# Performance work log

Hardware: AMD Instinct MI355X
Metric: run time of the kernel (lower is better)

The kernel has to match this reference:

```python
import jax, jax.numpy as jnp
import numpy as np

N = 8192; S = 32; EMB = 256; NH = 8; HD = EMB // NH; NT = 4; K = 2; L = 2; E = 131072
IN_DIMS = [128, 64, 32, 16]; COUNTS = [4096, 2048, 1024, 1024]
BETA = 1.0; TEMPER = 1.0; SLOPE = 0.2; LN_EPS = 1e-5


def setup_inputs() -> dict:
    key = jax.random.key(0)
    ks = iter(jax.random.split(key, 64))
    def nrm(shape, scale=1.0):
        return jax.random.normal(next(ks), shape, jnp.float32) * scale
    inp = {}
    for i, (d, c) in enumerate(zip(IN_DIMS, COUNTS)):
        inp[f"feat{i}"] = nrm((c, d))
        inp[f"Wfc{i}"] = nrm((d, EMB), d ** -0.5)
        inp[f"bfc{i}"] = nrm((EMB,), 0.01)
    inp["type_emb"] = nrm((NT, NT))
    inp["Wgcn"] = nrm((K, EMB, EMB), EMB ** -0.5)
    inp["bgcn"] = nrm((K, EMB), 0.01)
    inp["Wre"] = nrm((K, NT, NT), NT ** -0.5)
    inp["bre"] = nrm((K, NT), 0.01)
    inp["wtre"] = jnp.ones((K, NT), jnp.float32)
    inp["Wl"] = nrm((L, EMB, EMB), EMB ** -0.5)
    inp["Wr"] = nrm((L, EMB, EMB), EMB ** -0.5)
    inp["al"] = nrm((L, HD), HD ** -0.5)
    inp["ar"] = nrm((L, HD), HD ** -0.5)
    inp["Wrs"] = nrm((L, NT, NT * NH), NT ** -0.5)
    inp["Wrt"] = nrm((L, NT, NT * NH), NT ** -0.5)
    inp["Wfin"] = nrm((L, EMB, EMB), EMB ** -0.5)
    inp["ln_g"] = jnp.ones((L, EMB), jnp.float32)
    inp["ln_b"] = jnp.zeros((L, EMB), jnp.float32)
    inp["src"] = jax.random.randint(next(ks), (E,), 0, N)
    inp["dst"] = jax.random.randint(next(ks), (E,), 0, N)
    inp["node_type"] = jnp.concatenate([jnp.full((c,), t, jnp.int32) for t, c in enumerate(COUNTS)])
    inp["seqs"] = jax.random.randint(next(ks), (N, S), 0, N)
    return inp


def _l2n(x):
    return x / jnp.maximum(jnp.linalg.norm(x, axis=1, keepdims=True), 1e-12)


def _ln(x, g, b):
    m = x.mean(-1, keepdims=True)
    v = ((x - m) ** 2).mean(-1, keepdims=True)
    return (x - m) * jax.lax.rsqrt(v + LN_EPS) * g + b


def _agt(h, rh, Wl_, Wr_, al_, ar_, Wrs_, Wrt_, Wfin_, g_, b_):
    B, Sq, _ = h.shape
    fl = (h @ Wl_).reshape(B, Sq, NH, HD).transpose(0, 2, 1, 3)  # [B,NH,S,HD]
    fr = (h @ Wr_).reshape(B, Sq, NH, HD).transpose(0, 2, 1, 3)
    sl = jnp.einsum('bhsd,d->bhs', jax.nn.leaky_relu(fl, SLOPE), al_)
    sr = jnp.einsum('bhsd,d->bhs', jax.nn.leaky_relu(fr, SLOPE), ar_)
    score = sl[:, :, :, None] + sr[:, :, None, :]  # [B,NH,S,S]
    rk = (rh @ Wrs_).reshape(B, Sq, NH, NT).transpose(0, 2, 1, 3)  # [B,NH,S,NT]
    rq = (rh @ Wrt_).reshape(B, Sq, NH, NT).transpose(0, 2, 1, 3)
    score = score + BETA * jnp.einsum('bhir,bhjr->bhij', rk, rq)
    attn = jax.nn.softmax(score / TEMPER, axis=-1)
    ctx = jnp.einsum('bhij,bhjd->bhid', attn, fr)
    h_sa = ctx.transpose(0, 2, 1, 3).reshape(B, Sq, EMB)
    return _ln(h + h_sa @ Wfin_, g_, b_)


def reference(feat0, feat1, feat2, feat3, Wfc0, bfc0, Wfc1, bfc1, Wfc2, bfc2, Wfc3, bfc3,
              type_emb, Wgcn, bgcn, Wre, bre, wtre, Wl, Wr, al, ar, Wrs, Wrt, Wfin, ln_g, ln_b,
              src, dst, node_type, seqs):
    feats = [feat0, feat1, feat2, feat3]
    Wfcs = [Wfc0, Wfc1, Wfc2, Wfc3]
    bfcs = [bfc0, bfc1, bfc2, bfc3]
    gh = jnp.concatenate([f @ W + b for f, W, b in zip(feats, Wfcs, bfcs)], axis=0)  # [N,EMB]
    Nn = gh.shape[0]
    loop = jnp.arange(Nn, dtype=src.dtype)  # self-loops (graph.add_self_loop)
    src_f = jnp.concatenate([src, loop]); dst_f = jnp.concatenate([dst, loop])
    ones = jnp.ones(src_f.shape[0], jnp.float32)
    outdeg = jnp.clip(jax.ops.segment_sum(ones, src_f, num_segments=Nn), 1.0)
    indeg = jnp.clip(jax.ops.segment_sum(ones, dst_f, num_segments=Nn), 1.0)
    n_out = outdeg ** -0.5; n_in = indeg ** -0.5
    ret = [_l2n(gh)]
    R = type_emb[node_type]  # [N,NT]
    for k in range(K):
        # GraphConv, norm='both', relu
        x = (gh * n_out[:, None]) @ Wgcn[k]
        gh = jax.nn.relu(jax.ops.segment_sum(x[src_f], dst_f, num_segments=Nn) * n_in[:, None] + bgcn[k])
        # REConv: left norm, weight, per-node type scale, scatter-sum, right norm, bias, relu
        r = ((R * n_out[:, None]) @ Wre[k]) * wtre[k][node_type][:, None]
        R = jax.nn.relu(jax.ops.segment_sum(r[src_f], dst_f, num_segments=Nn) * n_in[:, None] + bre[k])
    h = gh[seqs]   # [N,S,EMB]
    rh = R[seqs]   # [N,S,NT]
    for l in range(L):
        h = _agt(h, rh, Wl[l], Wr[l], al[l], ar[l], Wrs[l], Wrt[l], Wfin[l], ln_g[l], ln_b[l])
        ret.append(_l2n(h[:, 0, :]))
    return jnp.concatenate(ret, axis=1)  # [N, EMB*(1+L)]
```

## Files before the change

### kernel.cpp

```cpp
#include <hip/hip_runtime.h>
#include <hip/hip_bf16.h>
#include <cstdint>
#include <cstddef>

typedef unsigned short ushortT;
typedef unsigned int uintT;

using bf16x8 = __attribute__((ext_vector_type(8))) short;
using f32x4  = __attribute__((ext_vector_type(4))) float;

static constexpr int NN  = 8192;
static constexpr int EE  = 131072;
static constexpr float SLOPE  = 0.2f;
static constexpr float LN_EPS = 1e-5f;

#define DEVI __device__ __forceinline__

DEVI float red32(float v) {
  #pragma unroll
  for (int m = 16; m >= 1; m >>= 1) v += __shfl_xor(v, m, 64);
  return v;
}
DEVI float red64(float v) {
  #pragma unroll
  for (int m = 32; m >= 1; m >>= 1) v += __shfl_xor(v, m, 64);
  return v;
}
DEVI float max32(float v) {
  #pragma unroll
  for (int m = 16; m >= 1; m >>= 1) v = fmaxf(v, __shfl_xor(v, m, 64));
  return v;
}
DEVI float blo(uintT u) { union { uintT i; float f; } c; c.i = u << 16; return c.f; }
DEVI float bhi(uintT u) { union { uintT i; float f; } c; c.i = u & 0xffff0000u; return c.f; }
DEVI float b2f(ushortT u) { union { uintT i; float f; } c; c.i = ((uintT)u) << 16; return c.f; }
DEVI ushortT f2bu(float f) {
  __hip_bfloat16 h = __float2bfloat16(f);
  return *reinterpret_cast<ushortT*>(&h);
}
DEVI void storeC(float* p, float v) { *p = v; }
DEVI void storeC(ushortT* p, float v) { *p = f2bu(v); }

__global__ __launch_bounds__(256) void fc_kernel(
    const float* __restrict__ f0, const float* __restrict__ f1,
    const float* __restrict__ f2, const float* __restrict__ f3,
    const float* __restrict__ w0, const float* __restrict__ w1,
    const float* __restrict__ w2, const float* __restrict__ w3,
    const float* __restrict__ b0, const float* __restrict__ b1,
    const float* __restrict__ b2, const float* __restrict__ b3,
    float* __restrict__ gh, float* __restrict__ out)
{
  const int nb = blockIdx.x * 32;
  const int t  = threadIdx.x;
  int base, D;
  const float *F, *W, *Bv;
  if (nb < 4096)      { base = 0;    D = 128; F = f0; W = w0; Bv = b0; }
  else if (nb < 6144) { base = 4096; D = 64;  F = f1; W = w1; Bv = b1; }
  else if (nb < 7168) { base = 6144; D = 32;  F = f2; W = w2; Bv = b2; }
  else                { base = 7168; D = 16;  F = f3; W = w3; Bv = b3; }

  __shared__ float Fs[32 * 128];
  __shared__ float red[32][4];
  __shared__ float nrm[32];

  const int total = 32 * D;
  for (int i = t; i < total; i += 256) Fs[i] = F[(size_t)(nb - base) * D + i];
  __syncthreads();

  float acc[32];
  #pragma unroll
  for (int r = 0; r < 32; ++r) acc[r] = Bv[t];
  for (int d = 0; d < D; ++d) {
    float w = W[(size_t)d * 256 + t];
    #pragma unroll
    for (int r = 0; r < 32; ++r) acc[r] = fmaf(Fs[r * D + d], w, acc[r]);
  }

  const int lane = t & 63, wid = t >> 6;
  #pragma unroll
  for (int r = 0; r < 32; ++r) {
    float v = acc[r] * acc[r];
    for (int o = 32; o > 0; o >>= 1) v += __shfl_down(v, o, 64);
    if (lane == 0) red[r][wid] = v;
  }
  __syncthreads();
  if (t < 32) {
    float s = red[t][0] + red[t][1] + red[t][2] + red[t][3];
    nrm[t] = 1.0f / fmaxf(sqrtf(s), 1e-12f);
  }
  __syncthreads();
  #pragma unroll
  for (int r = 0; r < 32; ++r) {
    gh[(size_t)(nb + r) * 256 + t]  = acc[r];
    out[(size_t)(nb + r) * 768 + t] = acc[r] * nrm[r];
  }
}

__global__ __launch_bounds__(256) void zero_counts(int* outc, int* inc) {
  int g = blockIdx.x * 256 + threadIdx.x;
  if (g < NN) outc[g] = 0; else inc[g - NN] = 0;
}
__global__ __launch_bounds__(256) void count_deg(const int* __restrict__ src,
                                                 const int* __restrict__ dst,
                                                 int* outc, int* inc) {
  int g = blockIdx.x * 256 + threadIdx.x;
  atomicAdd(&outc[src[g]], 1);
  atomicAdd(&inc[dst[g]], 1);
}
__global__ __launch_bounds__(1024) void scan_kernel(
    const int* __restrict__ inc, const int* __restrict__ outc,
    int* __restrict__ offs, int* __restrict__ cur,
    float* __restrict__ n_out, float* __restrict__ n_in)
{
  __shared__ int sums[1024];
  const int t = threadIdx.x;
  int x[8];
  const int base = t * 8;
  int s = 0;
  #pragma unroll
  for (int i = 0; i < 8; ++i) { int v = inc[base + i] + 1; x[i] = s; s += v; }
  sums[t] = s;
  __syncthreads();
  for (int off = 1; off < 1024; off <<= 1) {
    int a = (t >= off) ? sums[t - off] : 0;
    __syncthreads();
    sums[t] += a;
    __syncthreads();
  }
  const int pre = (t > 0) ? sums[t - 1] : 0;
  #pragma unroll
  for (int i = 0; i < 8; ++i) {
    const int o = pre + x[i];
    offs[base + i] = o;
    cur[base + i]  = o;
    n_in[base + i]  = rsqrtf((float)inc[base + i] + 1.0f);
    n_out[base + i] = rsqrtf((float)outc[base + i] + 1.0f);
  }
  if (t == 1023) offs[NN] = sums[1023];
}
__global__ __launch_bounds__(256) void fill_csr(const int* __restrict__ src,
                                                const int* __restrict__ dst,
                                                int* cur, int* __restrict__ csr) {
  int g = blockIdx.x * 256 + threadIdx.x;
  int s, d;
  if (g < EE) { s = src[g]; d = dst[g]; }
  else        { s = g - EE; d = g - EE; }
  int pos = atomicAdd(&cur[d], 1);
  csr[pos] = s;
}
__global__ __launch_bounds__(256) void init_R(const float* __restrict__ type_emb,
                                              const int* __restrict__ nt,
                                              float* __restrict__ R) {
  int g = blockIdx.x * 256 + threadIdx.x;
  int n = g >> 2, c = g & 3;
  R[g] = type_emb[nt[n] * 4 + c];
}

template<bool ROWSCALE, bool STORE, bool RED, typename CT>
__global__ __launch_bounds__(256) void mfma_gemm_kernel(
    const float* __restrict__ A, const float* __restrict__ W,
    const float* __restrict__ rowscale,
    CT* __restrict__ C, const float* __restrict__ avec,
    float* __restrict__ SSo)
{
  const int m0 = blockIdx.x * 64;
  const int n0 = blockIdx.y * 64;
  const int t = threadIdx.x;
  const int w = t >> 6, l = t & 63;
  const int wr = w >> 1, wc = w & 1;
  const int l15 = l & 15, l16 = l >> 4;

  __shared__ alignas(16) ushortT As[64][72];
  __shared__ alignas(16) ushortT Bs[64][72];

  f32x4 acc[2][2];
  #pragma unroll
  for (int mh = 0; mh < 2; ++mh)
    #pragma unroll
    for (int nh = 0; nh < 2; ++nh)
      #pragma unroll
      for (int r = 0; r < 4; ++r) acc[mh][nh][r] = 0.f;

  for (int k0 = 0; k0 < 256; k0 += 64) {
    #pragma unroll
    for (int rep = 0; rep < 16; ++rep) {
      int flat = rep * 256 + t;
      int r = flat >> 6, k = flat & 63;
      float v = A[(size_t)(m0 + r) * 256 + k0 + k];
      if constexpr (ROWSCALE) v *= rowscale[m0 + r];
      As[r][k] = f2bu(v);
    }
    #pragma unroll
    for (int rep = 0; rep < 16; ++rep) {
      int flat = rep * 256 + t;
      int k = flat >> 6, n = flat & 63;
      Bs[n][k] = f2bu(W[(size_t)(k0 + k) * 256 + n0 + n]);
    }
    __syncthreads();
    #pragma unroll
    for (int ks = 0; ks < 2; ++ks) {
      const int kb = ks * 32 + l16 * 8;
      bf16x8 afr[2], bfr[2];
      #pragma unroll
      for (int mh = 0; mh < 2; ++mh)
        afr[mh] = *reinterpret_cast<const bf16x8*>(&As[wr * 32 + mh * 16 + l15][kb]);
      #pragma unroll
      for (int nh = 0; nh < 2; ++nh)
        bfr[nh] = *reinterpret_cast<const bf16x8*>(&Bs[wc * 32 + nh * 16 + l15][kb]);
      #pragma unroll
      for (int mh = 0; mh < 2; ++mh)
        #pragma unroll
        for (int nh = 0; nh < 2; ++nh)
          acc[mh][nh] = __builtin_amdgcn_mfma_f32_16x16x32_bf16(
              afr[mh], bfr[nh], acc[mh][nh], 0, 0, 0);
    }
    __syncthreads();
  }
  if constexpr (STORE) {
    #pragma unroll
    for (int mh = 0; mh < 2; ++mh)
      #pragma unroll
      for (int nh = 0; nh < 2; ++nh)
        #pragma unroll
        for (int r = 0; r < 4; ++r) {
          const int row = m0 + wr * 32 + mh * 16 + l16 * 4 + r;
          const int col = n0 + wc * 32 + nh * 16 + l15;
          storeC(&C[(size_t)row * 256 + col], acc[mh][nh][r]);
        }
  }
  if constexpr (RED) {
    const float av0 = avec[l15], av1 = avec[16 + l15];
    #pragma unroll
    for (int mh = 0; mh < 2; ++mh)
      #pragma unroll
      for (int r = 0; r < 4; ++r) {
        float s = 0.f;
        {
          float x = acc[mh][0][r];
          s = fmaf(x > 0.f ? x : SLOPE * x, av0, s);
          x = acc[mh][1][r];
          s = fmaf(x > 0.f ? x : SLOPE * x, av1, s);
        }
        #pragma unroll
        for (int m = 8; m >= 1; m >>= 1) s += __shfl_xor(s, m, 64);
        if (l15 == 0) {
          const int row = m0 + wr * 32 + mh * 16 + l16 * 4 + r;
          SSo[(size_t)row * 8 + blockIdx.y * 2 + wc] = s;
        }
      }
  }
}

__global__ __launch_bounds__(256) void mfma_wlwr_kernel(
    const float* __restrict__ A,
    const float* __restrict__ Wl_, const float* __restrict__ Wr_,
    float* __restrict__ GR1,
    const float* __restrict__ al_, const float* __restrict__ ar_,
    float* __restrict__ SL, float* __restrict__ SR)
{
  const int m0 = blockIdx.x * 64;
  const int n0 = blockIdx.y * 64;
  const int t = threadIdx.x;
  const int w = t >> 6, l = t & 63;
  const int wr = w >> 1, wc = w & 1;
  const int l15 = l & 15, l16 = l >> 4;

  __shared__ alignas(16) ushortT As[64][72];
  __shared__ alignas(16) ushortT Bl[64][72];
  __shared__ alignas(16) ushortT Br[64][72];

  f32x4 accl[2][2], accr[2][2];
  #pragma unroll
  for (int mh = 0; mh < 2; ++mh)
    #pragma unroll
    for (int nh = 0; nh < 2; ++nh)
      #pragma unroll
      for (int r = 0; r < 4; ++r) { accl[mh][nh][r] = 0.f; accr[mh][nh][r] = 0.f; }

  for (int k0 = 0; k0 < 256; k0 += 64) {
    #pragma unroll
    for (int rep = 0; rep < 16; ++rep) {
      int flat = rep * 256 + t;
      int r = flat >> 6, k = flat & 63;
      As[r][k] = f2bu(A[(size_t)(m0 + r) * 256 + k0 + k]);
    }
    #pragma unroll
    for (int rep = 0; rep < 16; ++rep) {
      int flat = rep * 256 + t;
      int k = flat >> 6, n = flat & 63;
      Bl[n][k] = f2bu(Wl_[(size_t)(k0 + k) * 256 + n0 + n]);
      Br[n][k] = f2bu(Wr_[(size_t)(k0 + k) * 256 + n0 + n]);
    }
    __syncthreads();
    #pragma unroll
    for (int ks = 0; ks < 2; ++ks) {
      const int kb = ks * 32 + l16 * 8;
      bf16x8 afr[2], blr[2], brr[2];
      #pragma unroll
      for (int mh = 0; mh < 2; ++mh)
        afr[mh] = *reinterpret_cast<const bf16x8*>(&As[wr * 32 + mh * 16 + l15][kb]);
      #pragma unroll
      for (int nh = 0; nh < 2; ++nh) {
        blr[nh] = *reinterpret_cast<const bf16x8*>(&Bl[wc * 32 + nh * 16 + l15][kb]);
        brr[nh] = *reinterpret_cast<const bf16x8*>(&Br[wc * 32 + nh * 16 + l15][kb]);
      }
      #pragma unroll
      for (int mh = 0; mh < 2; ++mh)
        #pragma unroll
        for (int nh = 0; nh < 2; ++nh) {
          accl[mh][nh] = __builtin_amdgcn_mfma_f32_16x16x32_bf16(
              afr[mh], blr[nh], accl[mh][nh], 0, 0, 0);
          accr[mh][nh] = __builtin_amdgcn_mfma_f32_16x16x32_bf16(
              afr[mh], brr[nh], accr[mh][nh], 0, 0, 0);
        }
    }
    __syncthreads();
  }
  #pragma unroll
  for (int mh = 0; mh < 2; ++mh)
    #pragma unroll
    for (int nh = 0; nh < 2; ++nh)
      #pragma unroll
      for (int r = 0; r < 4; ++r) {
        const int row = m0 + wr * 32 + mh * 16 + l16 * 4 + r;
        const int col = n0 + wc * 32 + nh * 16 + l15;
        GR1[(size_t)row * 256 + col] = accr[mh][nh][r];
      }
  const float al0 = al_[l15], al1 = al_[16 + l15];
  const float ar0 = ar_[l15], ar1 = ar_[16 + l15];
  #pragma unroll
  for (int mh = 0; mh < 2; ++mh)
    #pragma unroll
    for (int r = 0; r < 4; ++r) {
      float sl = 0.f, sr = 0.f;
      {
        float x = accl[mh][0][r];
        sl = fmaf(x > 0.f ? x : SLOPE * x, al0, sl);
        x = accl[mh][1][r];
        sl = fmaf(x > 0.f ? x : SLOPE * x, al1, sl);
        x = accr[mh][0][r];
        sr = fmaf(x > 0.f ? x : SLOPE * x, ar0, sr);
        x = accr[mh][1][r];
        sr = fmaf(x > 0.f ? x : SLOPE * x, ar1, sr);
      }
      #pragma unroll
      for (int m = 8; m >= 1; m >>= 1) {
        sl += __shfl_xor(sl, m, 64);
        sr += __shfl_xor(sr, m, 64);
      }
      if (l15 == 0) {
        const int row = m0 + wr * 32 + mh * 16 + l16 * 4 + r;
        SL[(size_t)row * 8 + blockIdx.y * 2 + wc] = sl;
        SR[(size_t)row * 8 + blockIdx.y * 2 + wc] = sr;
      }
    }
}

__global__ __launch_bounds__(256) void agg2_kernel(
    const int* __restrict__ offs, const int* __restrict__ csr,
    const ushortT* __restrict__ X, const float* __restrict__ n_in,
    const float* __restrict__ bias, float* __restrict__ ghn,
    ushortT* __restrict__ ghb)
{
  const int n  = blockIdx.x * 2 + (threadIdx.x >> 7);
  const int tc = threadIdx.x & 127;
  const uintT* X2 = reinterpret_cast<const uintT*>(X);
  const int s0 = offs[n], s1 = offs[n + 1];
  float a0 = 0.f, a1 = 0.f;
  for (int i = s0; i < s1; ++i) {
    const uintT u = X2[(size_t)csr[i] * 128 + tc];
    a0 += blo(u);
    a1 += bhi(u);
  }
  const float ni = n_in[n];
  const float g0 = fmaxf(fmaf(a0, ni, bias[2 * tc]), 0.f);
  const float g1 = fmaxf(fmaf(a1, ni, bias[2 * tc + 1]), 0.f);
  float2 g2; g2.x = g0; g2.y = g1;
  reinterpret_cast<float2*>(ghn)[(size_t)n * 128 + tc] = g2;
  if (ghb)
    reinterpret_cast<uintT*>(ghb)[(size_t)n * 128 + tc] =
        (uintT)f2bu(g0) | ((uintT)f2bu(g1) << 16);
}

__global__ __launch_bounds__(256) void re_proj(
    const float* __restrict__ R, const float* __restrict__ n_out,
    const float* __restrict__ Wre, const float* __restrict__ wtre,
    const int* __restrict__ nt, float* __restrict__ rtmp)
{
  int g = blockIdx.x * 256 + threadIdx.x;
  int n = g >> 2, j = g & 3;
  float s = 0.f;
  #pragma unroll
  for (int c = 0; c < 4; ++c) s += R[n * 4 + c] * Wre[c * 4 + j];
  rtmp[g] = s * n_out[n] * wtre[nt[n]];
}
__global__ __launch_bounds__(256) void re_agg(
    const int* __restrict__ offs, const int* __restrict__ csr,
    const float* __restrict__ rtmp, const float* __restrict__ n_in,
    const float* __restrict__ bre, float* __restrict__ Rn)
{
  int g = blockIdx.x * 256 + threadIdx.x;
  int n = g >> 2, j = g & 3;
  float a = 0.f;
  for (int i = offs[n]; i < offs[n + 1]; ++i) a += rtmp[csr[i] * 4 + j];
  Rn[g] = fmaxf(fmaf(a, n_in[n], bre[j]), 0.f);
}
__global__ __launch_bounds__(256) void rkq_kernel(
    const float* __restrict__ R, const float* __restrict__ Wrs,
    const float* __restrict__ Wrt, float* __restrict__ RKQ)
{
  int g = blockIdx.x * 256 + threadIdx.x;
  int n = g >> 7, c = g & 127;
  int which = c >> 5, cc = c & 31;
  const float* Wp = (which == 0) ? Wrs : (which == 1) ? Wrt
                   : (which == 2) ? (Wrs + 128) : (Wrt + 128);
  float s = 0.f;
  #pragma unroll
  for (int r = 0; r < 4; ++r) s += R[n * 4 + r] * Wp[r * 32 + cc];
  RKQ[g] = s;
}

__global__ __launch_bounds__(256) void vec4_kernel(
    const float* __restrict__ ln_g, const float* __restrict__ ln_b,
    const float* __restrict__ Wr2, float* __restrict__ vecs)
{
  const int which = blockIdx.x, t = threadIdx.x;
  const float* s = (which & 1) ? ln_b : ln_g;
  float a = 0.f;
  for (int k = 0; k < 256; ++k) a = fmaf(s[k], Wr2[(size_t)k * 256 + t], a);
  vecs[which * 256 + t] = a;
}
__global__ __launch_bounds__(256) void wg2i_kernel(
    const float* __restrict__ ln_g, const float* __restrict__ Wr2,
    ushortT* __restrict__ Wg2i)
{
  const int gid = blockIdx.x * 256 + threadIdx.x;
  const int ks  = gid >> 10;
  const int cgl = (gid >> 6) & 15;
  const int l   = gid & 63;
  const int col = cgl * 16 + (l & 15);
  const int kb  = ks * 32 + (l >> 4) * 8;
  ushortT v[8];
  #pragma unroll
  for (int e = 0; e < 8; ++e)
    v[e] = f2bu(ln_g[kb + e] * Wr2[(size_t)(kb + e) * 256 + col]);
  *reinterpret_cast<bf16x8*>(&Wg2i[(size_t)gid * 8]) =
      *reinterpret_cast<const bf16x8*>(v);
}
__global__ __launch_bounds__(256) void wl2b_kernel(
    const float* __restrict__ Wl2, ushortT* __restrict__ Wl2b)
{
  int g = blockIdx.x * 256 + threadIdx.x;
  Wl2b[g] = f2bu(Wl2[g]);
}

__global__ __launch_bounds__(256) void mega7_kernel(
    const int* __restrict__ seqs,
    const ushortT* __restrict__ ghb,
    const ushortT* __restrict__ GW,
    const float* __restrict__ SLg, const float* __restrict__ SRg,
    const float* __restrict__ RKQ,
    const float* __restrict__ vecs,
    const ushortT* __restrict__ Wg2i,
    const ushortT* __restrict__ Wl2b,
    const float* __restrict__ al2, const float* __restrict__ ar2,
    const float* __restrict__ ln_g, const float* __restrict__ ln_b,
    float* __restrict__ h1r0buf, float* __restrict__ ctx2buf,
    float* __restrict__ out)
{
  __shared__ int idx[32];
  __shared__ alignas(16) ushortT bufA[10240];
  __shared__ alignas(16) ushortT bufB[10240];
  __shared__ float SRs[8][32];
  __shared__ float RQs[32][36];
  __shared__ float rk2s[32];
  __shared__ float part[32][4], partq[32][4];
  __shared__ float mu_s[32], rs_s[32];
  __shared__ float SR2s[8][32];
  __shared__ float sl2s[8];
  __shared__ float scp[8][32];
  __shared__ float h1r0s[256];
  __shared__ float wred4[4];
  __shared__ float nrm1s;

  const int b = blockIdx.x, t = threadIdx.x;
  const int h8 = t >> 5, lo = t & 31;
  const int w = t >> 6, l = t & 63;
  const int l15 = l & 15, l16 = l >> 4;

  if (t < 32) idx[t] = seqs[b * 32 + t];
  __syncthreads();

  const float sli = SLg[(size_t)idx[lo] * 8 + h8];
  const float rk0 = RKQ[(size_t)idx[lo] * 128 + h8 * 4 + 0];
  const float rk1 = RKQ[(size_t)idx[lo] * 128 + h8 * 4 + 1];
  const float rk2_ = RKQ[(size_t)idx[lo] * 128 + h8 * 4 + 2];
  const float rk3 = RKQ[(size_t)idx[lo] * 128 + h8 * 4 + 3];

  {
    const uintT* GWu = reinterpret_cast<const uintT*>(GW);
    #pragma unroll
    for (int rep = 0; rep < 16; ++rep) {
      int flat = rep * 256 + t;
      int j = flat >> 7, cp = flat & 127;
      const uintT u = GWu[(size_t)idx[j] * 128 + cp];
      const int rA = 2 * cp;
      const int k = (rA >> 3) & 3;
      const int off = (((j >> 3) ^ k) << 3) + (j & 7);
      bufA[rA * 40 + off]       = (ushortT)(u & 0xffffu);
      bufA[(rA + 1) * 40 + off] = (ushortT)(u >> 16);
    }
  }
  SRs[h8][lo] = SRg[(size_t)idx[lo] * 8 + h8];
  #pragma unroll
  for (int rep = 0; rep < 4; ++rep) {
    int flat = rep * 256 + t, s3 = flat >> 5, c3 = flat & 31;
    RQs[s3][c3] = RKQ[(size_t)idx[s3] * 128 + 32 + c3];
  }
  if (t < 32) rk2s[t] = RKQ[(size_t)idx[0] * 128 + 64 + t];
  __syncthreads();

  {
    float p1[32];
    float m = -1e30f;
    #pragma unroll
    for (int j = 0; j < 32; ++j) {
      float sc = sli + SRs[h8][j]
               + rk0 * RQs[j][h8 * 4 + 0] + rk1 * RQs[j][h8 * 4 + 1]
               + rk2_ * RQs[j][h8 * 4 + 2] + rk3 * RQs[j][h8 * 4 + 3];
      p1[j] = sc; m = fmaxf(m, sc);
    }
    float sum = 0.f;
    #pragma unroll
    for (int j = 0; j < 32; ++j) { p1[j] = __expf(p1[j] - m); sum += p1[j]; }
    const float inv = 1.f / sum;
    const int row = t;
    const int k = (row >> 3) & 3;
    uintT* pw = reinterpret_cast<uintT*>(bufB) + row * 20;
    #pragma unroll
    for (int o = 0; o < 4; ++o) {
      uint4 v;
      v.x = (uintT)f2bu(p1[8 * o + 0] * inv) | ((uintT)f2bu(p1[8 * o + 1] * inv) << 16);
      v.y = (uintT)f2bu(p1[8 * o + 2] * inv) | ((uintT)f2bu(p1[8 * o + 3] * inv) << 16);
      v.z = (uintT)f2bu(p1[8 * o + 4] * inv) | ((uintT)f2bu(p1[8 * o + 5] * inv) << 16);
      v.w = (uintT)f2bu(p1[8 * o + 6] * inv) | ((uintT)f2bu(p1[8 * o + 7] * inv) << 16);
      *reinterpret_cast<uint4*>(pw + ((o ^ k) << 2)) = v;
    }
  }
  __syncthreads();

  int irow[2][4];
  #pragma unroll
  for (int mh = 0; mh < 2; ++mh)
    #pragma unroll
    for (int r = 0; r < 4; ++r)
      irow[mh][r] = idx[mh * 16 + l16 * 4 + r];

  bf16x8 af[2][2];
  #pragma unroll
  for (int hh = 0; hh < 2; ++hh) {
    const int h = 2 * w + hh;
    #pragma unroll
    for (int mh = 0; mh < 2; ++mh) {
      const int row = h * 32 + mh * 16 + l15;
      const int k = (row >> 3) & 3;
      af[hh][mh] = *reinterpret_cast<const bf16x8*>(&bufB[row * 40 + ((l16 ^ k) << 3)]);
    }
  }

  f32x4 acc[2][2][2];
  #pragma unroll
  for (int hh = 0; hh < 2; ++hh) {
    const int h = 2 * w + hh;
    bf16x8 bf[2];
    #pragma unroll
    for (int nh = 0; nh < 2; ++nh) {
      const int row = h * 32 + nh * 16 + l15;
      const int k = (row >> 3) & 3;
      bf[nh] = *reinterpret_cast<const bf16x8*>(&bufA[row * 40 + ((l16 ^ k) << 3)]);
    }
    #pragma unroll
    for (int mh = 0; mh < 2; ++mh)
      #pragma unroll
      for (int nh = 0; nh < 2; ++nh) {
        f32x4 z = {0.f, 0.f, 0.f, 0.f};
        acc[hh][mh][nh] = __builtin_amdgcn_mfma_f32_16x16x32_bf16(af[hh][mh], bf[nh], z, 0, 0, 0);
      }
  }
  {
    float sum_[2][4], sq_[2][4];
    #pragma unroll
    for (int mh = 0; mh < 2; ++mh)
      #pragma unroll
      for (int r = 0; r < 4; ++r) { sum_[mh][r] = 0.f; sq_[mh][r] = 0.f; }
    #pragma unroll
    for (int hh = 0; hh < 2; ++hh)
      #pragma unroll
      for (int mh = 0; mh < 2; ++mh)
        #pragma unroll
        for (int nh = 0; nh < 2; ++nh) {
          const int col = (2 * w + hh) * 32 + nh * 16 + l15;
          #pragma unroll
          for (int r = 0; r < 4; ++r) {
            float v = acc[hh][mh][nh][r] + b2f(ghb[(size_t)irow[mh][r] * 256 + col]);
            acc[hh][mh][nh][r] = v;
            sum_[mh][r] += v;
            sq_[mh][r] = fmaf(v, v, sq_[mh][r]);
          }
        }
    #pragma unroll
    for (int mh = 0; mh < 2; ++mh)
      #pragma unroll
      for (int r = 0; r < 4; ++r) {
        float s = sum_[mh][r], q = sq_[mh][r];
        #pragma unroll
        for (int m = 8; m >= 1; m >>= 1) {
          s += __shfl_xor(s, m, 64);
          q += __shfl_xor(q, m, 64);
        }
        if (l15 == 0) {
          part[mh * 16 + l16 * 4 + r][w]  = s;
          partq[mh * 16 + l16 * 4 + r][w] = q;
        }
      }
    if (l16 == 0) {
      #pragma unroll
      for (int hh = 0; hh < 2; ++hh)
        #pragma unroll
        for (int nh = 0; nh < 2; ++nh)
          h1r0s[(2 * w + hh) * 32 + nh * 16 + l15] = acc[hh][0][nh][0];
    }
  }
  __syncthreads();

  if (t < 32) {
    float sm = part[t][0] + part[t][1] + part[t][2] + part[t][3];
    float sq = partq[t][0] + partq[t][1] + partq[t][2] + partq[t][3];
    const float m = sm * (1.f / 256.f);
    const float v = fmaxf(sq * (1.f / 256.f) - m * m, 0.f);
    mu_s[t] = m;
    rs_s[t] = rsqrtf(v + LN_EPS);
  }
  __syncthreads();

  #pragma unroll
  for (int hh = 0; hh < 2; ++hh)
    #pragma unroll
    for (int mh = 0; mh < 2; ++mh)
      #pragma unroll
      for (int nh = 0; nh < 2; ++nh) {
        const int col = (2 * w + hh) * 32 + nh * 16 + l15;
        #pragma unroll
        for (int r = 0; r < 4; ++r) {
          const int row = mh * 16 + l16 * 4 + r;
          bufB[row * 264 + col] = f2bu(acc[hh][mh][nh][r]);
        }
      }
  #pragma unroll
  for (int rep = 0; rep < 4; ++rep) {
    int flat = rep * 256 + t, s3 = flat >> 5, c3 = flat & 31;
    RQs[s3][c3] = RKQ[(size_t)idx[s3] * 128 + 96 + c3];
  }
  {
    const float mu0 = mu_s[0], rs0 = rs_s[0];
    float hv = fmaf((h1r0s[t] - mu0) * rs0, ln_g[t], ln_b[t]);
    h1r0buf[(size_t)b * 256 + t] = hv;
    float sq = red64(hv * hv);
    h1r0s[t] = hv;
    if ((t & 63) == 0) wred4[t >> 6] = sq;
  }
  __syncthreads();

  if (t == 0) nrm1s = 1.f / fmaxf(sqrtf(wred4[0] + wred4[1] + wred4[2] + wred4[3]), 1e-12f);

  {
    f32x4 acc2[2][4];
    #pragma unroll
    for (int mh = 0; mh < 2; ++mh)
      #pragma unroll
      for (int cg = 0; cg < 4; ++cg)
        #pragma unroll
        for (int r = 0; r < 4; ++r) acc2[mh][cg][r] = 0.f;
    #pragma unroll
    for (int ks = 0; ks < 8; ++ks) {
      const int ko = ks * 32 + l16 * 8;
      bf16x8 a2[2];
      #pragma unroll
      for (int mh = 0; mh < 2; ++mh)
        a2[mh] = *reinterpret_cast<const bf16x8*>(&bufB[(mh * 16 + l15) * 264 + ko]);
      #pragma unroll
      for (int cg = 0; cg < 4; ++cg) {
        const bf16x8 b2 = *reinterpret_cast<const bf16x8*>(
            &Wg2i[((size_t)(ks * 16 + (w * 4 + cg)) * 64 + l) * 8]);
        #pragma unroll
        for (int mh = 0; mh < 2; ++mh)
          acc2[mh][cg] = __builtin_amdgcn_mfma_f32_16x16x32_bf16(a2[mh], b2, acc2[mh][cg], 0, 0, 0);
      }
    }
    float rsv[2][4], rmv[2][4];
    #pragma unroll
    for (int mh = 0; mh < 2; ++mh)
      #pragma unroll
      for (int r = 0; r < 4; ++r) {
        const int row = mh * 16 + l16 * 4 + r;
        rsv[mh][r] = rs_s[row];
        rmv[mh][r] = rsv[mh][r] * mu_s[row];
      }
    float sacc[2][2][4];
    #pragma unroll
    for (int hh = 0; hh < 2; ++hh)
      #pragma unroll
      for (int mh = 0; mh < 2; ++mh)
        #pragma unroll
        for (int r = 0; r < 4; ++r) sacc[hh][mh][r] = 0.f;
    float ar2v[2] = { ar2[l15], ar2[16 + l15] };
    #pragma unroll
    for (int cg = 0; cg < 4; ++cg) {
      const int col = w * 64 + cg * 16 + l15;
      const float v1c = vecs[col], v2c = vecs[256 + col];
      const int hh = cg >> 1;
      #pragma unroll
      for (int mh = 0; mh < 2; ++mh)
        #pragma unroll
        for (int r = 0; r < 4; ++r) {
          const int row = mh * 16 + l16 * 4 + r;
          float fa = fmaf(rsv[mh][r], acc2[mh][cg][r], fmaf(-rmv[mh][r], v1c, v2c));
          bufA[row * 268 + col] = f2bu(fa);
          float lr = fa > 0.f ? fa : SLOPE * fa;
          sacc[hh][mh][r] = fmaf(lr, ar2v[cg & 1], sacc[hh][mh][r]);
        }
    }
    #pragma unroll
    for (int hh = 0; hh < 2; ++hh)
      #pragma unroll
      for (int mh = 0; mh < 2; ++mh)
        #pragma unroll
        for (int r = 0; r < 4; ++r) {
          float s = sacc[hh][mh][r];
          #pragma unroll
          for (int m = 8; m >= 1; m >>= 1) s += __shfl_xor(s, m, 64);
          if (l15 == 0) SR2s[2 * w + hh][mh * 16 + l16 * 4 + r] = s;
        }
  }
  {
    float fl = 0.f;
    #pragma unroll 8
    for (int k = 0; k < 256; ++k)
      fl = fmaf(h1r0s[k], b2f(Wl2b[(size_t)k * 256 + t]), fl);
    float lr = (fl > 0.f ? fl : SLOPE * fl) * al2[lo];
    lr = red32(lr);
    if (lo == 0) sl2s[h8] = lr;
  }
  __syncthreads();

  {
    float s2 = sl2s[h8] + SR2s[h8][lo]
             + rk2s[h8 * 4 + 0] * RQs[lo][h8 * 4 + 0]
             + rk2s[h8 * 4 + 1] * RQs[lo][h8 * 4 + 1]
             + rk2s[h8 * 4 + 2] * RQs[lo][h8 * 4 + 2]
             + rk2s[h8 * 4 + 3] * RQs[lo][h8 * 4 + 3];
    const float m2 = max32(s2);
    const float e = __expf(s2 - m2);
    const float su = red32(e);
    scp[h8][lo] = e / su;
  }
  __syncthreads();

  {
    float a = 0.f;
    #pragma unroll
    for (int j = 0; j < 32; ++j) a = fmaf(scp[h8][j], b2f(bufA[j * 268 + t]), a);
    ctx2buf[(size_t)b * 256 + t] = a;
  }
  out[(size_t)b * 768 + 256 + t] = h1r0s[t] * nrm1s;
}

__global__ __launch_bounds__(256) void ln_l2n_kernel(
    const float* __restrict__ Y, const float* __restrict__ res,
    const float* __restrict__ lng, const float* __restrict__ lnb,
    float* __restrict__ out)
{
  const int row = blockIdx.x, t = threadIdx.x;
  __shared__ float s4[4], q4[4];
  const float y = Y[(size_t)row * 256 + t] + res[(size_t)row * 256 + t];
  float s = red64(y);
  float q = red64(y * y);
  if ((t & 63) == 0) { s4[t >> 6] = s; q4[t >> 6] = q; }
  __syncthreads();
  const float mu = (s4[0] + s4[1] + s4[2] + s4[3]) * (1.f / 256.f);
  const float var = fmaxf((q4[0] + q4[1] + q4[2] + q4[3]) * (1.f / 256.f) - mu * mu, 0.f);
  const float rstd = rsqrtf(var + LN_EPS);
  const float yn = fmaf((y - mu) * rstd, lng[t], lnb[t]);
  float nq = red64(yn * yn);
  __syncthreads();
  if ((t & 63) == 0) s4[t >> 6] = nq;
  __syncthreads();
  const float nrm = 1.f / fmaxf(sqrtf(s4[0] + s4[1] + s4[2] + s4[3]), 1e-12f);
  out[(size_t)row * 768 + 512 + t] = yn * nrm;
}

extern "C" void kernel_launch(void* const* d_in, const int* in_sizes, int n_in,
                              void* d_out, int out_size, void* d_ws, size_t ws_size,
                              hipStream_t stream)
{
  (void)in_sizes; (void)n_in; (void)out_size; (void)ws_size;

  const float* feat[4]; const float* wfc[4]; const float* bfc[4];
  for (int i = 0; i < 4; ++i) {
    feat[i] = (const float*)d_in[i * 3 + 0];
    wfc[i]  = (const float*)d_in[i * 3 + 1];
    bfc[i]  = (const float*)d_in[i * 3 + 2];
  }
  const float* type_emb = (const float*)d_in[12];
  const float* Wgcn = (const float*)d_in[13];
  const float* bgcn = (const float*)d_in[14];
  const float* Wre  = (const float*)d_in[15];
  const float* bre  = (const float*)d_in[16];
  const float* wtre = (const float*)d_in[17];
  const float* Wl   = (const float*)d_in[18];
  const float* Wr   = (const float*)d_in[19];
  const float* al   = (const float*)d_in[20];
  const float* ar   = (const float*)d_in[21];
  const float* Wrs  = (const float*)d_in[22];
  const float* Wrt  = (const float*)d_in[23];
  const float* Wfin = (const float*)d_in[24];
  const float* ln_g = (const float*)d_in[25];
  const float* ln_b = (const float*)d_in[26];
  const int* src       = (const int*)d_in[27];
  const int* dst       = (const int*)d_in[28];
  const int* node_type = (const int*)d_in[29];
  const int* seqs      = (const int*)d_in[30];
  float* out = (float*)d_out;

  char* p = (char*)d_ws;
  auto take = [&](size_t n) { char* q = p; p += (n + 255) & ~(size_t)255; return q; };
  float* gh    = (float*)take((size_t)NN * 256 * 4);
  float* Xf    = (float*)take((size_t)NN * 256 * 4);
  float* GR1   = (float*)take((size_t)NN * 256 * 4);
  float* RKQ   = (float*)take((size_t)NN * 128 * 4);
  float* SLg   = (float*)take((size_t)NN * 8 * 4);
  float* SRg   = (float*)take((size_t)NN * 8 * 4);
  float* n_out = (float*)take((size_t)NN * 4);
  float* n_in_ = (float*)take((size_t)NN * 4);
  int*   outc  = (int*)take((size_t)NN * 4);
  int*   inc   = (int*)take((size_t)NN * 4);
  int*   offs  = (int*)take((size_t)(NN + 1) * 4);
  int*   cur   = (int*)take((size_t)NN * 4);
  int*   csr   = (int*)take((size_t)(EE + NN) * 4);
  float* R     = (float*)take((size_t)NN * 4 * 4);
  float* rtmp  = (float*)take((size_t)NN * 4 * 4);
  ushortT* GW   = (ushortT*)take((size_t)NN * 256 * 2);
  ushortT* ghb  = (ushortT*)take((size_t)NN * 256 * 2);
  ushortT* Xb   = (ushortT*)take((size_t)NN * 256 * 2);
  ushortT* Wg2i = (ushortT*)take((size_t)131072 * 2);
  ushortT* Wl2b = (ushortT*)take((size_t)65536 * 2);
  float* vecs  = (float*)take((size_t)2 * 256 * 4);
  float* ctx2buf = Xf;
  float* h1r0buf = GR1;
  float* Yb      = gh;

  const float* Wr2 = Wr + 65536;
  const float* Wl2 = Wl + 65536;

  fc_kernel<<<256, 256, 0, stream>>>(feat[0], feat[1], feat[2], feat[3],
                                     wfc[0], wfc[1], wfc[2], wfc[3],
                                     bfc[0], bfc[1], bfc[2], bfc[3], gh, out);
  zero_counts<<<64, 256, 0, stream>>>(outc, inc);
  count_deg<<<512, 256, 0, stream>>>(src, dst, outc, inc);
  scan_kernel<<<1, 1024, 0, stream>>>(inc, outc, offs, cur, n_out, n_in_);
  fill_csr<<<544, 256, 0, stream>>>(src, dst, cur, csr);
  init_R<<<128, 256, 0, stream>>>(type_emb, node_type, R);

  vec4_kernel<<<2, 256, 0, stream>>>(ln_g, ln_b, Wr2, vecs);
  wg2i_kernel<<<64, 256, 0, stream>>>(ln_g, Wr2, Wg2i);
  wl2b_kernel<<<256, 256, 0, stream>>>(Wl2, Wl2b);

  for (int k = 0; k < 2; ++k) {
    mfma_gemm_kernel<true, true, false, ushortT>
        <<<dim3(128, 4), 256, 0, stream>>>(gh, Wgcn + (size_t)k * 65536,
                                           n_out, Xb, nullptr, nullptr);
    agg2_kernel<<<NN / 2, 256, 0, stream>>>(offs, csr, Xb, n_in_,
                                            bgcn + k * 256, gh,
                                            k == 1 ? ghb : nullptr);
    re_proj<<<128, 256, 0, stream>>>(R, n_out, Wre + k * 16, wtre + k * 4, node_type, rtmp);
    re_agg<<<128, 256, 0, stream>>>(offs, csr, rtmp, n_in_, bre + k * 4, R);
  }

  rkq_kernel<<<4096, 256, 0, stream>>>(R, Wrs, Wrt, RKQ);
  mfma_wlwr_kernel<<<dim3(128, 4), 256, 0, stream>>>(
      gh, Wl, Wr, GR1, al, ar, SLg, SRg);
  mfma_gemm_kernel<false, true, false, ushortT>
      <<<dim3(128, 4), 256, 0, stream>>>(GR1, Wfin, nullptr, GW, nullptr, nullptr);

  mega7_kernel<<<NN, 256, 0, stream>>>(seqs, ghb, GW, SLg, SRg, RKQ, vecs,
                                       Wg2i, Wl2b,
                                       al + 32, ar + 32, ln_g, ln_b,
                                       h1r0buf, ctx2buf, out);

  mfma_gemm_kernel<false, true, false, float>
      <<<dim3(128, 4), 256, 0, stream>>>(ctx2buf, Wfin + 65536, nullptr,
                                         Yb, nullptr, nullptr);
  ln_l2n_kernel<<<NN, 256, 0, stream>>>(Yb, h1r0buf, ln_g + 256, ln_b + 256, out);
}
```

Before: 527.4 us.

## Compute layer-2 left projection of row 0 via MFMA with folded LayerNorm

```diff
diff --git a/kernel.cpp b/kernel.cpp
--- a/kernel.cpp
+++ b/kernel.cpp
@@ -422,17 +422,19 @@
 
 __global__ __launch_bounds__(256) void vec4_kernel(
     const float* __restrict__ ln_g, const float* __restrict__ ln_b,
-    const float* __restrict__ Wr2, float* __restrict__ vecs)
+    const float* __restrict__ Wr2, const float* __restrict__ Wl2,
+    float* __restrict__ vecs)
 {
   const int which = blockIdx.x, t = threadIdx.x;
+  const float* W = (which < 2) ? Wr2 : Wl2;
   const float* s = (which & 1) ? ln_b : ln_g;
   float a = 0.f;
-  for (int k = 0; k < 256; ++k) a = fmaf(s[k], Wr2[(size_t)k * 256 + t], a);
+  for (int k = 0; k < 256; ++k) a = fmaf(s[k], W[(size_t)k * 256 + t], a);
   vecs[which * 256 + t] = a;
 }
 __global__ __launch_bounds__(256) void wg2i_kernel(
-    const float* __restrict__ ln_g, const float* __restrict__ Wr2,
-    ushortT* __restrict__ Wg2i)
+    const float* __restrict__ ln_g, const float* __restrict__ W,
+    ushortT* __restrict__ Wi)
 {
   const int gid = blockIdx.x * 256 + threadIdx.x;
   const int ks  = gid >> 10;
@@ -443,18 +445,12 @@
   ushortT v[8];
   #pragma unroll
   for (int e = 0; e < 8; ++e)
-    v[e] = f2bu(ln_g[kb + e] * Wr2[(size_t)(kb + e) * 256 + col]);
-  *reinterpret_cast<bf16x8*>(&Wg2i[(size_t)gid * 8]) =
+    v[e] = f2bu(ln_g[kb + e] * W[(size_t)(kb + e) * 256 + col]);
+  *reinterpret_cast<bf16x8*>(&Wi[(size_t)gid * 8]) =
       *reinterpret_cast<const bf16x8*>(v);
 }
-__global__ __launch_bounds__(256) void wl2b_kernel(
-    const float* __restrict__ Wl2, ushortT* __restrict__ Wl2b)
-{
-  int g = blockIdx.x * 256 + threadIdx.x;
-  Wl2b[g] = f2bu(Wl2[g]);
-}
-
-__global__ __launch_bounds__(256) void mega7_kernel(
+
+__global__ __launch_bounds__(256) void mega9_kernel(
     const int* __restrict__ seqs,
     const ushortT* __restrict__ ghb,
     const ushortT* __restrict__ GW,
@@ -462,7 +458,7 @@
     const float* __restrict__ RKQ,
     const float* __restrict__ vecs,
     const ushortT* __restrict__ Wg2i,
-    const ushortT* __restrict__ Wl2b,
+    const ushortT* __restrict__ Wgl2i,
     const float* __restrict__ al2, const float* __restrict__ ar2,
     const float* __restrict__ ln_g, const float* __restrict__ ln_b,
     float* __restrict__ h1r0buf, float* __restrict__ ctx2buf,
@@ -477,7 +473,7 @@
   __shared__ float part[32][4], partq[32][4];
   __shared__ float mu_s[32], rs_s[32];
   __shared__ float SR2s[8][32];
-  __shared__ float sl2s[8];
+  __shared__ float sl2p[8][2];
   __shared__ float scp[8][32];
   __shared__ float h1r0s[256];
   __shared__ float wred4[4];
@@ -675,12 +671,17 @@
 
   {
     f32x4 acc2[2][4];
+    f32x4 acc3[4];
     #pragma unroll
     for (int mh = 0; mh < 2; ++mh)
       #pragma unroll
       for (int cg = 0; cg < 4; ++cg)
         #pragma unroll
         for (int r = 0; r < 4; ++r) acc2[mh][cg][r] = 0.f;
+    #pragma unroll
+    for (int cg = 0; cg < 4; ++cg)
+      #pragma unroll
+      for (int r = 0; r < 4; ++r) acc3[cg][r] = 0.f;
     #pragma unroll
     for (int ks = 0; ks < 8; ++ks) {
       const int ko = ks * 32 + l16 * 8;
@@ -690,11 +691,13 @@
         a2[mh] = *reinterpret_cast<const bf16x8*>(&bufB[(mh * 16 + l15) * 264 + ko]);
       #pragma unroll
       for (int cg = 0; cg < 4; ++cg) {
-        const bf16x8 b2 = *reinterpret_cast<const bf16x8*>(
-            &Wg2i[((size_t)(ks * 16 + (w * 4 + cg)) * 64 + l) * 8]);
+        const size_t bidx = ((size_t)(ks * 16 + (w * 4 + cg)) * 64 + l) * 8;
+        const bf16x8 b2 = *reinterpret_cast<const bf16x8*>(&Wg2i[bidx]);
         #pragma unroll
         for (int mh = 0; mh < 2; ++mh)
           acc2[mh][cg] = __builtin_amdgcn_mfma_f32_16x16x32_bf16(a2[mh], b2, acc2[mh][cg], 0, 0, 0);
+        const bf16x8 b3 = *reinterpret_cast<const bf16x8*>(&Wgl2i[bidx]);
+        acc3[cg] = __builtin_amdgcn_mfma_f32_16x16x32_bf16(a2[0], b3, acc3[cg], 0, 0, 0);
       }
     }
     float rsv[2][4], rmv[2][4];
@@ -741,20 +744,23 @@
           for (int m = 8; m >= 1; m >>= 1) s += __shfl_xor(s, m, 64);
           if (l15 == 0) SR2s[2 * w + hh][mh * 16 + l16 * 4 + r] = s;
         }
-  }
+    if (l16 == 0) {
+      const float rs0 = rs_s[0], rm0 = rs_s[0] * mu_s[0];
+      #pragma unroll
+      for (int cg = 0; cg < 4; ++cg) {
+        const int col = w * 64 + cg * 16 + l15;
+        float fl = fmaf(rs0, acc3[cg][0], fmaf(-rm0, vecs[512 + col], vecs[768 + col]));
+        float lr = (fl > 0.f ? fl : SLOPE * fl) * al2[col & 31];
+        #pragma unroll
+        for (int m = 8; m >= 1; m >>= 1) lr += __shfl_xor(lr, m, 64);
+        if (l15 == 0) sl2p[(w * 4 + cg) >> 1][cg & 1] = lr;
+      }
+    }
+  }
+  __syncthreads();
+
   {
-    float fl = 0.f;
-    #pragma unroll 8
-    for (int k = 0; k < 256; ++k)
-      fl = fmaf(h1r0s[k], b2f(Wl2b[(size_t)k * 256 + t]), fl);
-    float lr = (fl > 0.f ? fl : SLOPE * fl) * al2[lo];
-    lr = red32(lr);
-    if (lo == 0) sl2s[h8] = lr;
-  }
-  __syncthreads();
-
-  {
-    float s2 = sl2s[h8] + SR2s[h8][lo]
+    float s2 = sl2p[h8][0] + sl2p[h8][1] + SR2s[h8][lo]
              + rk2s[h8 * 4 + 0] * RQs[lo][h8 * 4 + 0]
              + rk2s[h8 * 4 + 1] * RQs[lo][h8 * 4 + 1]
              + rk2s[h8 * 4 + 2] * RQs[lo][h8 * 4 + 2]
@@ -849,12 +855,12 @@
   int*   csr   = (int*)take((size_t)(EE + NN) * 4);
   float* R     = (float*)take((size_t)NN * 4 * 4);
   float* rtmp  = (float*)take((size_t)NN * 4 * 4);
-  ushortT* GW   = (ushortT*)take((size_t)NN * 256 * 2);
-  ushortT* ghb  = (ushortT*)take((size_t)NN * 256 * 2);
-  ushortT* Xb   = (ushortT*)take((size_t)NN * 256 * 2);
-  ushortT* Wg2i = (ushortT*)take((size_t)131072 * 2);
-  ushortT* Wl2b = (ushortT*)take((size_t)65536 * 2);
-  float* vecs  = (float*)take((size_t)2 * 256 * 4);
+  ushortT* GW    = (ushortT*)take((size_t)NN * 256 * 2);
+  ushortT* ghb   = (ushortT*)take((size_t)NN * 256 * 2);
+  ushortT* Xb    = (ushortT*)take((size_t)NN * 256 * 2);
+  ushortT* Wg2i  = (ushortT*)take((size_t)65536 * 2);
+  ushortT* Wgl2i = (ushortT*)take((size_t)65536 * 2);
+  float* vecs  = (float*)take((size_t)4 * 256 * 4);
   float* ctx2buf = Xf;
   float* h1r0buf = GR1;
   float* Yb      = gh;
@@ -871,9 +877,9 @@
   fill_csr<<<544, 256, 0, stream>>>(src, dst, cur, csr);
   init_R<<<128, 256, 0, stream>>>(type_emb, node_type, R);
 
-  vec4_kernel<<<2, 256, 0, stream>>>(ln_g, ln_b, Wr2, vecs);
-  wg2i_kernel<<<64, 256, 0, stream>>>(ln_g, Wr2, Wg2i);
-  wl2b_kernel<<<256, 256, 0, stream>>>(Wl2, Wl2b);
+  vec4_kernel<<<4, 256, 0, stream>>>(ln_g, ln_b, Wr2, Wl2, vecs);
+  wg2i_kernel<<<32, 256, 0, stream>>>(ln_g, Wr2, Wg2i);
+  wg2i_kernel<<<32, 256, 0, stream>>>(ln_g, Wl2, Wgl2i);
 
   for (int k = 0; k < 2; ++k) {
     mfma_gemm_kernel<true, true, false, ushortT>
@@ -892,8 +898,8 @@
   mfma_gemm_kernel<false, true, false, ushortT>
       <<<dim3(128, 4), 256, 0, stream>>>(GR1, Wfin, nullptr, GW, nullptr, nullptr);
 
-  mega7_kernel<<<NN, 256, 0, stream>>>(seqs, ghb, GW, SLg, SRg, RKQ, vecs,
-                                       Wg2i, Wl2b,
+  mega9_kernel<<<NN, 256, 0, stream>>>(seqs, ghb, GW, SLg, SRg, RKQ, vecs,
+                                       Wg2i, Wgl2i,
                                        al + 32, ar + 32, ln_g, ln_b,
                                        h1r0buf, ctx2buf, out);
 
```

Result: slower. 609.1 us (+15.5%).
